# Performance work log

Measured on AMD Instinct MI355X. Metric: run time of the kernel, lower is better.

## Reference

```python
import jax, jax.numpy as jnp
import numpy as np

B, TQ, TKV, D, H = 2, 1024, 1024, 1024, 16
HD = D // H
BUCKETS, MAX_REL = 32, 128
SPAN = BUCKETS  # pos_ebd_size


def make_log_bucket_position(rel_pos, bucket_size, max_position):
    sign = jnp.sign(rel_pos)
    mid = bucket_size // 2
    abs_pos = jnp.where((rel_pos < mid) & (rel_pos > -mid), mid - 1, jnp.abs(rel_pos))
    log_pos = jnp.ceil(jnp.log(abs_pos.astype(jnp.float32) / mid)
                       / np.float32(np.log((max_position - 1) / mid)) * (mid - 1)) + mid
    return jnp.where(abs_pos <= mid, rel_pos, (log_pos * sign).astype(rel_pos.dtype))


def setup_inputs():
    key = jax.random.key(0)
    ks = jax.random.split(key, 12)
    s = 0.02
    f32 = jnp.float32
    return {
        "query_states": jax.random.normal(ks[0], (B, TQ, D), f32),
        "key_value_states": jax.random.normal(ks[1], (B, TKV, D), f32),
        "Wq": jax.random.normal(ks[2], (D, D), f32) * s, "bq": jnp.zeros((D,), f32),
        "Wk": jax.random.normal(ks[3], (D, D), f32) * s, "bk": jnp.zeros((D,), f32),
        "Wv": jax.random.normal(ks[4], (D, D), f32) * s, "bv": jnp.zeros((D,), f32),
        "Wo": jax.random.normal(ks[5], (D, D), f32) * s, "bo": jnp.zeros((D,), f32),
        "Wpk": jax.random.normal(ks[6], (D, D), f32) * s, "bpk": jnp.zeros((D,), f32),
        "Wpq": jax.random.normal(ks[7], (D, D), f32) * s, "bpq": jnp.zeros((D,), f32),
        "rel_emb": jax.random.normal(ks[8], (2 * SPAN, D), f32) * s,
        "ln_g": jnp.ones((D,), f32), "ln_b": jnp.zeros((D,), f32),
        "attention_mask": jnp.zeros((B, TKV), jnp.bool_),
    }


def reference(query_states, key_value_states, Wq, bq, Wk, bk, Wv, bv, Wo, bo,
              Wpk, bpk, Wpq, bpq, rel_emb, ln_g, ln_b, attention_mask):
    # projections -> [B,H,T,hd]
    q = (query_states @ Wq.T + bq).reshape(B, TQ, H, HD).transpose(0, 2, 1, 3)
    k = (key_value_states @ Wk.T + bk).reshape(B, TKV, H, HD).transpose(0, 2, 1, 3)
    v = (key_value_states @ Wv.T + bv).reshape(B, TKV, H, HD).transpose(0, 2, 1, 3)
    scale = jnp.sqrt(jnp.float32(HD * 3))  # scale_factor = 1 + c2p + p2c
    scores = jnp.einsum('bhqd,bhkd->bhqk', q, k) / scale

    # layer-normalized relative embeddings [2*SPAN, D]
    mu = rel_emb.mean(-1, keepdims=True)
    var = ((rel_emb - mu) ** 2).mean(-1, keepdims=True)
    re = (rel_emb - mu) * jax.lax.rsqrt(var + 1e-5) * ln_g + ln_b
    pos_k = (re @ Wpk.T + bpk).reshape(2 * SPAN, H, HD).transpose(1, 0, 2)  # [H,2S,hd]
    pos_q = (re @ Wpq.T + bpq).reshape(2 * SPAN, H, HD).transpose(1, 0, 2)

    rel = make_log_bucket_position(jnp.arange(TQ)[:, None] - jnp.arange(TKV)[None, :],
                                   BUCKETS, MAX_REL)                      # [Tq,Tkv]
    c2p_pos = jnp.clip(rel + SPAN, 0, 2 * SPAN - 1)
    p2c_pos = jnp.clip(-rel + SPAN, 0, 2 * SPAN - 1)
    pscale = jnp.sqrt(jnp.float32(HD * 2))

    # c2p: gather along relative-position axis
    c2p = jnp.einsum('bhqd,hpd->bhqp', q, pos_k)                          # [B,H,Tq,2S]
    iq = jnp.arange(TQ)[:, None]
    c2p_g = c2p[:, :, iq, c2p_pos]                                        # [B,H,Tq,Tkv]

    # p2c: gather then transpose (requires Tq == Tkv, as in original torch expand)
    p2c = jnp.einsum('bhkd,hpd->bhkp', k, pos_q)                          # [B,H,Tkv,2S]
    ik = jnp.arange(TKV)[:, None]
    p2c_g = p2c[:, :, ik, p2c_pos].transpose(0, 1, 3, 2)                  # [B,H,Tq,Tkv]

    scores = scores + c2p_g / pscale + p2c_g / pscale
    scores = jnp.where(attention_mask[:, None, None, :], -jnp.inf, scores)
    probs = jax.nn.softmax(scores.astype(jnp.float32), axis=-1).astype(q.dtype)

    ctx = jnp.einsum('bhqk,bhkd->bhqd', probs, v).transpose(0, 2, 1, 3).reshape(B, TQ, D)
    return ctx @ Wo.T + bo
```

## Files before the change

### kernel.cpp

```cpp
#include <hip/hip_runtime.h>
#include <hip/hip_bf16.h>
#include <math.h>

#define B   2
#define TQ  1024
#define TKV 1024
#define D   1024
#define H   16
#define HD  64
#define P   64
#define SPAN 32

#define NEG_INF (-3.0e38f)

typedef __attribute__((ext_vector_type(8))) short bf16x8;
typedef __attribute__((ext_vector_type(4))) float f32x4;
typedef unsigned short ushort_t;

static constexpr size_t QF_OFF   = 0;
static constexpr size_t RE_OFF   = (size_t)2 * 1024 * 1024;
static constexpr size_t POSK_OFF = RE_OFF + (size_t)64 * 1024;
static constexpr size_t POSQ_OFF = POSK_OFF + (size_t)64 * 1024;
static constexpr size_t FLOATS_END = POSQ_OFF + (size_t)64 * 1024;
static constexpr size_t SHORT_BASE_BYTES = FLOATS_END * 4;
static constexpr size_t C2P_S  = 0;
static constexpr size_t P2C_S  = (size_t)2 * 1024 * 1024;
static constexpr size_t KH_S   = (size_t)4 * 1024 * 1024;
static constexpr size_t KL_S   = (size_t)6 * 1024 * 1024;
static constexpr size_t VTH_S  = (size_t)8 * 1024 * 1024;
static constexpr size_t VTL_S  = (size_t)10 * 1024 * 1024;
static constexpr size_t CTXH_S = (size_t)12 * 1024 * 1024;
static constexpr size_t CTXL_S = (size_t)14 * 1024 * 1024;
static constexpr size_t TAB_OFF_BYTES = SHORT_BASE_BYTES + (size_t)16 * 1024 * 1024 * 2;

__device__ __forceinline__ void split2(float x, unsigned short& h, unsigned short& l) {
  unsigned int u = __float_as_uint(x);
  h = (unsigned short)(u >> 16);
  float r = x - __uint_as_float(u & 0xffff0000u);
  unsigned int v = __float_as_uint(r);
  v += 0x7fffu + ((v >> 16) & 1u);
  l = (unsigned short)(v >> 16);
}

__device__ __forceinline__ unsigned short bf16rn(float x) {
  unsigned int v = __float_as_uint(x);
  v += 0x7fffu + ((v >> 16) & 1u);
  return (unsigned short)(v >> 16);
}

__device__ __forceinline__ float bf2f(unsigned short u) {
  return __uint_as_float(((unsigned int)u) << 16);
}

__global__ __launch_bounds__(256) void ln_kernel(const float* __restrict__ x,
    const float* __restrict__ g, const float* __restrict__ bta, float* __restrict__ out) {
  const int row = blockIdx.x;
  const float* xr = x + (size_t)row * D;
  const int tid = threadIdx.x;
  __shared__ float red[4];
  float s = 0.f;
  for (int i = tid; i < D; i += 256) s += xr[i];
  #pragma unroll
  for (int off = 32; off; off >>= 1) s += __shfl_down(s, off);
  if ((tid & 63) == 0) red[tid >> 6] = s;
  __syncthreads();
  float mu = (red[0] + red[1] + red[2] + red[3]) * (1.0f / D);
  __syncthreads();
  float vs = 0.f;
  for (int i = tid; i < D; i += 256) { float dd = xr[i] - mu; vs += dd * dd; }
  #pragma unroll
  for (int off = 32; off; off >>= 1) vs += __shfl_down(vs, off);
  if ((tid & 63) == 0) red[tid >> 6] = vs;
  __syncthreads();
  float var = (red[0] + red[1] + red[2] + red[3]) * (1.0f / D);
  float rs = rsqrtf(var + 1e-5f);
  for (int i = tid; i < D; i += 256)
    out[(size_t)row * D + i] = (xr[i] - mu) * rs * g[i] + bta[i];
}

__global__ void tab_kernel(unsigned char* __restrict__ tab) {
  int i = blockIdx.x * 256 + threadIdx.x;
  if (i >= 2047) return;
  int d = i - 1023;
  int ad = d < 0 ? -d : d;
  int bucket;
  if (ad <= 16) {
    bucket = d;
  } else {
    double x = log((double)ad / 16.0) / log(127.0 / 16.0) * 15.0;
    double xr = floor(x + 0.5);
    double xc = (fabs(x - xr) < 1e-9) ? xr : ceil(x);
    int li = (int)xc + 16;
    bucket = (d > 0) ? li : -li;
  }
  int t = bucket + SPAN;
  t = t < 0 ? 0 : (t > 63 ? 63 : t);
  tab[i] = (unsigned char)t;
}

__global__ __launch_bounds__(256) void gemm_pos(const float* __restrict__ A,
    const float* __restrict__ W0, const float* __restrict__ b0, float* __restrict__ C0,
    const float* __restrict__ W1, const float* __restrict__ b1, float* __restrict__ C1) {
  const float* W = blockIdx.z ? W1 : W0;
  const float* bias = blockIdx.z ? b1 : b0;
  float* C = blockIdx.z ? C1 : C0;

  __shared__ short sAh[64 * 32], sAl[64 * 32], sBh[64 * 32], sBl[64 * 32];
  const int t = threadIdx.x;
  const int bn = blockIdx.x * 64;
  const int wid = t >> 6, lane = t & 63;
  const int wr = wid >> 1, wc = wid & 1;
  const int fr = lane & 15, fo = (lane >> 4) * 8;
  const int srow = t >> 3, scol = (t & 7) * 4;

  f32x4 acc[2][2];
  #pragma unroll
  for (int i = 0; i < 2; i++)
    #pragma unroll
    for (int j = 0; j < 2; j++) acc[i][j] = (f32x4){0.f, 0.f, 0.f, 0.f};

  float4 rA[2], rW[2];
  auto ld = [&](int k0) {
    #pragma unroll
    for (int i = 0; i < 2; i++) {
      rA[i] = *(const float4*)&A[(size_t)(srow + 32 * i) * 1024 + k0 + scol];
      rW[i] = *(const float4*)&W[(size_t)(bn + srow + 32 * i) * 1024 + k0 + scol];
    }
  };
  ld(0);

  for (int k0 = 0; k0 < 1024; k0 += 32) {
    __syncthreads();
    #pragma unroll
    for (int i = 0; i < 2; i++) {
      int row = srow + 32 * i;
      unsigned short h0,h1,h2,h3,l0,l1,l2,l3;
      split2(rA[i].x,h0,l0); split2(rA[i].y,h1,l1); split2(rA[i].z,h2,l2); split2(rA[i].w,h3,l3);
      *(short4*)&sAh[row * 32 + scol] = make_short4((short)h0,(short)h1,(short)h2,(short)h3);
      *(short4*)&sAl[row * 32 + scol] = make_short4((short)l0,(short)l1,(short)l2,(short)l3);
      split2(rW[i].x,h0,l0); split2(rW[i].y,h1,l1); split2(rW[i].z,h2,l2); split2(rW[i].w,h3,l3);
      *(short4*)&sBh[row * 32 + scol] = make_short4((short)h0,(short)h1,(short)h2,(short)h3);
      *(short4*)&sBl[row * 32 + scol] = make_short4((short)l0,(short)l1,(short)l2,(short)l3);
    }
    if (k0 + 32 < 1024) ld(k0 + 32);
    __syncthreads();

    bf16x8 ah[2], al[2], bh[2], bl[2];
    #pragma unroll
    for (int mf = 0; mf < 2; mf++) {
      int r = (wr * 32 + mf * 16 + fr) * 32 + fo;
      ah[mf] = *(const bf16x8*)&sAh[r];
      al[mf] = *(const bf16x8*)&sAl[r];
    }
    #pragma unroll
    for (int nf = 0; nf < 2; nf++) {
      int r = (wc * 32 + nf * 16 + fr) * 32 + fo;
      bh[nf] = *(const bf16x8*)&sBh[r];
      bl[nf] = *(const bf16x8*)&sBl[r];
    }
    #pragma unroll
    for (int mf = 0; mf < 2; mf++)
      #pragma unroll
      for (int nf = 0; nf < 2; nf++) {
        acc[mf][nf] = __builtin_amdgcn_mfma_f32_16x16x32_bf16(ah[mf], bh[nf], acc[mf][nf], 0, 0, 0);
        acc[mf][nf] = __builtin_amdgcn_mfma_f32_16x16x32_bf16(ah[mf], bl[nf], acc[mf][nf], 0, 0, 0);
        acc[mf][nf] = __builtin_amdgcn_mfma_f32_16x16x32_bf16(al[mf], bh[nf], acc[mf][nf], 0, 0, 0);
      }
  }

  #pragma unroll
  for (int mf = 0; mf < 2; mf++) {
    int rbase = wr * 32 + mf * 16 + (lane >> 4) * 4;
    #pragma unroll
    for (int nf = 0; nf < 2; nf++) {
      int col = bn + wc * 32 + nf * 16 + fr;
      float bb = bias[col];
      #pragma unroll
      for (int r = 0; r < 4; r++)
        C[(size_t)(rbase + r) * 1024 + col] = acc[mf][nf][r] + bb;
    }
  }
}

__global__ __launch_bounds__(256) void gemm_split(
    const float* __restrict__ A0, const float* __restrict__ A1, const float* __restrict__ A2,
    const float* __restrict__ W0, const float* __restrict__ W1, const float* __restrict__ W2,
    const float* __restrict__ b0, const float* __restrict__ b1, const float* __restrict__ b2,
    float* __restrict__ Cf0,
    ushort_t* __restrict__ KH_, ushort_t* __restrict__ KL_,
    ushort_t* __restrict__ VH_, ushort_t* __restrict__ VL_,
    int M, int N, int K) {
  const int z = blockIdx.z;
  const float* A = (z == 0) ? A0 : (z == 1) ? A1 : A2;
  const float* W = (z == 0) ? W0 : (z == 1) ? W1 : W2;
  const float* bias = (z == 0) ? b0 : (z == 1) ? b1 : b2;

  __shared__ short sAhi[128 * 32];
  __shared__ short sAlo[128 * 32];
  __shared__ short sBhi[64 * 32];
  __shared__ short sBlo[64 * 32];

  const int t = threadIdx.x;
  const int bm = blockIdx.y * 128, bn = blockIdx.x * 64;
  const int wid = t >> 6, lane = t & 63;
  const int wr = wid >> 1, wc = wid & 1;
  const int fr = lane & 15, fo = (lane >> 4) * 8;

  f32x4 acc[4][2];
  #pragma unroll
  for (int i = 0; i < 4; i++)
    #pragma unroll
    for (int j = 0; j < 2; j++)
      acc[i][j] = (f32x4){0.f, 0.f, 0.f, 0.f};

  const int srow = t >> 3;
  const int scol = (t & 7) * 4;

  float4 rA[4], rW[2];
  auto ld = [&](int k0) {
    #pragma unroll
    for (int i = 0; i < 4; i++)
      rA[i] = *(const float4*)&A[(size_t)(bm + srow + 32 * i) * K + k0 + scol];
    #pragma unroll
    for (int i = 0; i < 2; i++)
      rW[i] = *(const float4*)&W[(size_t)(bn + srow + 32 * i) * K + k0 + scol];
  };
  ld(0);

  for (int k0 = 0; k0 < K; k0 += 32) {
    __syncthreads();
    #pragma unroll
    for (int i = 0; i < 4; i++) {
      int row = srow + 32 * i;
      unsigned short h0, h1, h2, h3, l0, l1, l2, l3;
      split2(rA[i].x, h0, l0); split2(rA[i].y, h1, l1); split2(rA[i].z, h2, l2); split2(rA[i].w, h3, l3);
      *(short4*)&sAhi[row * 32 + scol] = make_short4((short)h0, (short)h1, (short)h2, (short)h3);
      *(short4*)&sAlo[row * 32 + scol] = make_short4((short)l0, (short)l1, (short)l2, (short)l3);
    }
    #pragma unroll
    for (int i = 0; i < 2; i++) {
      int row = srow + 32 * i;
      unsigned short h0, h1, h2, h3, l0, l1, l2, l3;
      split2(rW[i].x, h0, l0); split2(rW[i].y, h1, l1); split2(rW[i].z, h2, l2); split2(rW[i].w, h3, l3);
      *(short4*)&sBhi[row * 32 + scol] = make_short4((short)h0, (short)h1, (short)h2, (short)h3);
      *(short4*)&sBlo[row * 32 + scol] = make_short4((short)l0, (short)l1, (short)l2, (short)l3);
    }
    if (k0 + 32 < K) ld(k0 + 32);
    __syncthreads();

    bf16x8 ah[4], al[4], bh[2], bl[2];
    #pragma unroll
    for (int mf = 0; mf < 4; mf++) {
      int r = (wr * 64 + mf * 16 + fr) * 32 + fo;
      ah[mf] = *(const bf16x8*)&sAhi[r];
      al[mf] = *(const bf16x8*)&sAlo[r];
    }
    #pragma unroll
    for (int nf = 0; nf < 2; nf++) {
      int r = (wc * 32 + nf * 16 + fr) * 32 + fo;
      bh[nf] = *(const bf16x8*)&sBhi[r];
      bl[nf] = *(const bf16x8*)&sBlo[r];
    }
    #pragma unroll
    for (int mf = 0; mf < 4; mf++)
      #pragma unroll
      for (int nf = 0; nf < 2; nf++) {
        acc[mf][nf] = __builtin_amdgcn_mfma_f32_16x16x32_bf16(ah[mf], bh[nf], acc[mf][nf], 0, 0, 0);
        acc[mf][nf] = __builtin_amdgcn_mfma_f32_16x16x32_bf16(ah[mf], bl[nf], acc[mf][nf], 0, 0, 0);
        acc[mf][nf] = __builtin_amdgcn_mfma_f32_16x16x32_bf16(al[mf], bh[nf], acc[mf][nf], 0, 0, 0);
      }
  }

  if (z == 0) {
    #pragma unroll
    for (int mf = 0; mf < 4; mf++) {
      int rbase = bm + wr * 64 + mf * 16 + (lane >> 4) * 4;
      #pragma unroll
      for (int nf = 0; nf < 2; nf++) {
        int col = bn + wc * 32 + nf * 16 + fr;
        float bb = bias[col];
        #pragma unroll
        for (int r = 0; r < 4; r++)
          Cf0[(size_t)(rbase + r) * N + col] = acc[mf][nf][r] + bb;
      }
    }
  } else if (z == 1) {
    #pragma unroll
    for (int mf = 0; mf < 4; mf++) {
      int rbase = bm + wr * 64 + mf * 16 + (lane >> 4) * 4;
      #pragma unroll
      for (int nf = 0; nf < 2; nf++) {
        int col = bn + wc * 32 + nf * 16 + fr;
        float bb = bias[col];
        #pragma unroll
        for (int r = 0; r < 4; r++) {
          unsigned short hh, ll;
          split2(acc[mf][nf][r] + bb, hh, ll);
          KH_[(size_t)(rbase + r) * N + col] = hh;
          KL_[(size_t)(rbase + r) * N + col] = ll;
        }
      }
    }
  } else {
    #pragma unroll
    for (int mf = 0; mf < 4; mf++) {
      int m0 = bm + wr * 64 + mf * 16 + (lane >> 4) * 4;
      int bb2 = m0 >> 10, t0 = m0 & 1023;
      #pragma unroll
      for (int nf = 0; nf < 2; nf++) {
        int col = bn + wc * 32 + nf * 16 + fr;
        int hh = col >> 6, dd = col & 63;
        float bvv = bias[col];
        unsigned short h4[4], l4[4];
        #pragma unroll
        for (int r = 0; r < 4; r++) split2(acc[mf][nf][r] + bvv, h4[r], l4[r]);
        size_t dst = (((size_t)bb2 * 16 + hh) * 64 + dd) * 1024 + t0;
        *(short4*)&VH_[dst] = make_short4((short)h4[0], (short)h4[1], (short)h4[2], (short)h4[3]);
        *(short4*)&VL_[dst] = make_short4((short)l4[0], (short)l4[1], (short)l4[2], (short)l4[3]);
      }
    }
  }
}

__global__ __launch_bounds__(256) void gemm_out(
    const ushort_t* __restrict__ AH, const ushort_t* __restrict__ AL,
    const float* __restrict__ W, const float* __restrict__ bias, float* __restrict__ C) {
  __shared__ short sAh[64 * 32], sAl[64 * 32], sBh[64 * 32], sBl[64 * 32];
  const int t = threadIdx.x;
  const int bm = blockIdx.y * 64, bn = blockIdx.x * 64;
  const int wid = t >> 6, lane = t & 63;
  const int wr = wid >> 1, wc = wid & 1;
  const int fr = lane & 15, fo = (lane >> 4) * 8;
  const int arow = t >> 2, achk = (t & 3) * 8;
  const int srow = t >> 3, scol = (t & 7) * 4;

  f32x4 acc[2][2];
  #pragma unroll
  for (int i = 0; i < 2; i++)
    #pragma unroll
    for (int j = 0; j < 2; j++) acc[i][j] = (f32x4){0.f, 0.f, 0.f, 0.f};

  bf16x8 rAH, rAL;
  float4 rW[2];
  auto ld = [&](int k0) {
    rAH = *(const bf16x8*)&AH[(size_t)(bm + arow) * 1024 + k0 + achk];
    rAL = *(const bf16x8*)&AL[(size_t)(bm + arow) * 1024 + k0 + achk];
    #pragma unroll
    for (int i = 0; i < 2; i++)
      rW[i] = *(const float4*)&W[(size_t)(bn + srow + 32 * i) * 1024 + k0 + scol];
  };
  ld(0);

  for (int k0 = 0; k0 < 1024; k0 += 32) {
    __syncthreads();
    *(bf16x8*)&sAh[arow * 32 + achk] = rAH;
    *(bf16x8*)&sAl[arow * 32 + achk] = rAL;
    #pragma unroll
    for (int i = 0; i < 2; i++) {
      int row = srow + 32 * i;
      unsigned short h0,h1,h2,h3,l0,l1,l2,l3;
      split2(rW[i].x,h0,l0); split2(rW[i].y,h1,l1); split2(rW[i].z,h2,l2); split2(rW[i].w,h3,l3);
      *(short4*)&sBh[row * 32 + scol] = make_short4((short)h0,(short)h1,(short)h2,(short)h3);
      *(short4*)&sBl[row * 32 + scol] = make_short4((short)l0,(short)l1,(short)l2,(short)l3);
    }
    if (k0 + 32 < 1024) ld(k0 + 32);
    __syncthreads();

    bf16x8 ah[2], al[2], bh[2], bl[2];
    #pragma unroll
    for (int mf = 0; mf < 2; mf++) {
      int r = (wr * 32 + mf * 16 + fr) * 32 + fo;
      ah[mf] = *(const bf16x8*)&sAh[r];
      al[mf] = *(const bf16x8*)&sAl[r];
    }
    #pragma unroll
    for (int nf = 0; nf < 2; nf++) {
      int r = (wc * 32 + nf * 16 + fr) * 32 + fo;
      bh[nf] = *(const bf16x8*)&sBh[r];
      bl[nf] = *(const bf16x8*)&sBl[r];
    }
    #pragma unroll
    for (int mf = 0; mf < 2; mf++)
      #pragma unroll
      for (int nf = 0; nf < 2; nf++) {
        acc[mf][nf] = __builtin_amdgcn_mfma_f32_16x16x32_bf16(ah[mf], bh[nf], acc[mf][nf], 0, 0, 0);
        acc[mf][nf] = __builtin_amdgcn_mfma_f32_16x16x32_bf16(ah[mf], bl[nf], acc[mf][nf], 0, 0, 0);
        acc[mf][nf] = __builtin_amdgcn_mfma_f32_16x16x32_bf16(al[mf], bh[nf], acc[mf][nf], 0, 0, 0);
      }
  }

  #pragma unroll
  for (int mf = 0; mf < 2; mf++) {
    int rbase = bm + wr * 32 + mf * 16 + (lane >> 4) * 4;
    #pragma unroll
    for (int nf = 0; nf < 2; nf++) {
      int col = bn + wc * 32 + nf * 16 + fr;
      float bb = bias[col];
      #pragma unroll
      for (int r = 0; r < 4; r++)
        C[(size_t)(rbase + r) * 1024 + col] = acc[mf][nf][r] + bb;
    }
  }
}

__global__ __launch_bounds__(256) void relproj_kernel(
    const float* __restrict__ X0, const float* __restrict__ P0, ushort_t* __restrict__ O0,
    const ushort_t* __restrict__ XH1, const ushort_t* __restrict__ XL1,
    const float* __restrict__ P1, ushort_t* __restrict__ O1) {
  const int z = blockIdx.z;
  const float* POS = z ? P1 : P0;
  ushort_t* out = z ? O1 : O0;
  const int bh = blockIdx.y, b = bh >> 4, h = bh & 15;
  const int t0 = blockIdx.x * 64;
  __shared__ __align__(16) float sx[64][68];
  __shared__ __align__(16) float sp[64][68];
  const int tid = threadIdx.x;
  for (int i = tid; i < 4096; i += 256) {
    int r = i >> 6, d = i & 63;
    size_t idx = ((size_t)b * TQ + t0 + r) * D + h * HD + d;
    sx[d][r] = z ? (bf2f(XH1[idx]) + bf2f(XL1[idx])) : X0[idx];
    sp[d][r] = POS[(size_t)r * D + h * HD + d];
  }
  __syncthreads();
  const int tx = tid & 15, ty = tid >> 4;
  float acc[4][4] = {};
  for (int d = 0; d < 64; d++) {
    float4 a4 = *(const float4*)&sx[d][ty * 4];
    float4 b4 = *(const float4*)&sp[d][tx * 4];
    float av[4] = {a4.x, a4.y, a4.z, a4.w};
    float bv[4] = {b4.x, b4.y, b4.z, b4.w};
    #pragma unroll
    for (int i = 0; i < 4; i++)
      #pragma unroll
      for (int j = 0; j < 4; j++)
        acc[i][j] += av[i] * bv[j];
  }
  const float inv_ps = 0.08838834764831845f;
  #pragma unroll
  for (int i = 0; i < 4; i++)
    #pragma unroll
    for (int j = 0; j < 4; j++)
      out[((size_t)bh * TQ + t0 + ty * 4 + i) * P + tx * 4 + j] = bf16rn(acc[i][j] * inv_ps);
}

__global__ __launch_bounds__(256) void attn_mfma(
    const float* __restrict__ qb,
    const ushort_t* __restrict__ KH, const ushort_t* __restrict__ KL,
    const ushort_t* __restrict__ VTH, const ushort_t* __restrict__ VTL,
    const ushort_t* __restrict__ c2p, const ushort_t* __restrict__ p2c,
    const unsigned char* __restrict__ mask, const unsigned char* __restrict__ tab,
    ushort_t* __restrict__ CTXH, ushort_t* __restrict__ CTXL) {
  const int flat = blockIdx.y * gridDim.x + blockIdx.x;
  const int nid = (flat & 7) * 64 + (flat >> 3);
  const int bh = nid >> 4, b = bh >> 4, h = bh & 15;
  const int q0 = (nid & 15) * 64;

  const int tid = threadIdx.x;
  const int wid = tid >> 6, lane = tid & 63;
  const int g = lane >> 4, fr = lane & 15;

  __shared__ __align__(16) short sKh[4096], sKl[4096], sVh[4096], sVl[4096];
  __shared__ __align__(16) ushort_t sc2p[64][72];
  __shared__ __align__(16) ushort_t sp2c[64][72];
  __shared__ unsigned char stab[2048];
  __shared__ unsigned char smask[64];

  bf16x8 qh[2], ql[2];
  {
    const int qrow = q0 + wid * 16 + fr;
    const float* qp = qb + ((size_t)b * TQ + qrow) * D + h * HD + g * 8;
    #pragma unroll
    for (int ks = 0; ks < 2; ks++) {
      float4 x0 = *(const float4*)(qp + ks * 32);
      float4 x1 = *(const float4*)(qp + ks * 32 + 4);
      float xs[8] = {x0.x, x0.y, x0.z, x0.w, x1.x, x1.y, x1.z, x1.w};
      bf16x8 th, tl;
      #pragma unroll
      for (int j = 0; j < 8; j++) {
        unsigned short hh, ll;
        split2(xs[j], hh, ll);
        th[j] = (short)hh; tl[j] = (short)ll;
      }
      qh[ks] = th; ql[ks] = tl;
    }
  }

  const int sr = tid >> 2;
  const int sj0 = tid & 3;
  const int smf = sr >> 4, sfr = sr & 15;
  const int cb = (tid & 3) * 16;
  const int qloc = wid * 16 + fr;

  {
    const ushort_t* cp = c2p + ((size_t)bh * TQ + q0 + sr) * P + cb;
    *(bf16x8*)&sc2p[sr][cb]     = *(const bf16x8*)cp;
    *(bf16x8*)&sc2p[sr][cb + 8] = *(const bf16x8*)(cp + 8);
  }
  for (int i = tid; i < 2047; i += 256) stab[i] = tab[i];
  __syncthreads();
  const float c2p0  = bf2f(sc2p[qloc][0]);
  const float c2p63 = bf2f(sc2p[qloc][63]);

  f32x4 acc[4];
  #pragma unroll
  for (int nf = 0; nf < 4; nf++) acc[nf] = (f32x4){0.f, 0.f, 0.f, 0.f};
  float m_run = NEG_INF, l_run = 0.f;

  const float inv_s = 0.07216878364870323f;

  bf16x8 rKh[2], rKl[2], rVh[2], rVl[2], rP0, rP1;
  unsigned char rmask = 0;

  auto load_tile = [&](int kt) {
    const int k0n = kt * 64;
    const size_t kbase = ((size_t)b * TKV + k0n + sr) * D + h * HD;
    const size_t vbase = ((size_t)bh * HD + sr) * TKV + k0n;
    const ushort_t* pp = p2c + ((size_t)bh * TKV + k0n + sr) * P + cb;
    #pragma unroll
    for (int u = 0; u < 2; u++) {
      int jj = sj0 + u * 4;
      rKh[u] = *(const bf16x8*)(KH + kbase + jj * 8);
      rKl[u] = *(const bf16x8*)(KL + kbase + jj * 8);
      rVh[u] = *(const bf16x8*)(VTH + vbase + jj * 8);
      rVl[u] = *(const bf16x8*)(VTL + vbase + jj * 8);
    }
    rP0 = *(const bf16x8*)pp;
    rP1 = *(const bf16x8*)(pp + 8);
    if (tid < 64) rmask = mask[(size_t)b * TKV + k0n + tid];
  };

  load_tile(0);

  for (int kt = 0; kt < TKV / 64; kt++) {
    const int k0 = kt * 64;
    __syncthreads();
    #pragma unroll
    for (int u = 0; u < 2; u++) {
      int jj = sj0 + u * 4;
      int sub = smf * 8 + (jj >> 2) * 4 + (jj & 3);
      *(bf16x8*)&sKh[sub * 128 + sfr * 8] = rKh[u];
      *(bf16x8*)&sKl[sub * 128 + sfr * 8] = rKl[u];
      *(bf16x8*)&sVh[sub * 128 + sfr * 8] = rVh[u];
      *(bf16x8*)&sVl[sub * 128 + sfr * 8] = rVl[u];
    }
    *(bf16x8*)&sp2c[sr][cb]     = rP0;
    *(bf16x8*)&sp2c[sr][cb + 8] = rP1;
    if (tid < 64) smask[tid] = rmask;
    if (kt + 1 < TKV / 64) load_tile(kt + 1);
    __syncthreads();

    f32x4 st[4];
    #pragma unroll
    for (int mf = 0; mf < 4; mf++) st[mf] = (f32x4){0.f, 0.f, 0.f, 0.f};
    __builtin_amdgcn_s_setprio(1);
    #pragma unroll
    for (int mf = 0; mf < 4; mf++) {
      #pragma unroll
      for (int ks = 0; ks < 2; ks++) {
        bf16x8 kh = *(const bf16x8*)&sKh[(mf * 8 + ks * 4 + g) * 128 + fr * 8];
        bf16x8 kl = *(const bf16x8*)&sKl[(mf * 8 + ks * 4 + g) * 128 + fr * 8];
        st[mf] = __builtin_amdgcn_mfma_f32_16x16x32_bf16(kh, qh[ks], st[mf], 0, 0, 0);
        st[mf] = __builtin_amdgcn_mfma_f32_16x16x32_bf16(kh, ql[ks], st[mf], 0, 0, 0);
        st[mf] = __builtin_amdgcn_mfma_f32_16x16x32_bf16(kl, qh[ks], st[mf], 0, 0, 0);
      }
    }
    __builtin_amdgcn_s_setprio(0);

    const int dtile = q0 - k0;
    float pv[4][4];
    float lmax = NEG_INF;
    if (dtile >= 192 || dtile <= -192) {
      const int C = (dtile >= 192) ? 63 : 0;
      const float cbias = (dtile >= 192) ? c2p63 : c2p0;
      #pragma unroll
      for (int mf = 0; mf < 4; mf++) {
        #pragma unroll
        for (int rr = 0; rr < 4; rr++) {
          int kj = mf * 16 + g * 4 + rr;
          float v = st[mf][rr] * inv_s + (cbias + bf2f(sp2c[kj][C]));
          v = smask[kj] ? NEG_INF : v;
          pv[mf][rr] = v;
          lmax = fmaxf(lmax, v);
        }
      }
    } else {
      const int dq = q0 + qloc - k0 + 1023;
      const ushort_t* c2prow = &sc2p[qloc][0];
      #pragma unroll
      for (int mf = 0; mf < 4; mf++) {
        #pragma unroll
        for (int rr = 0; rr < 4; rr++) {
          int kj = mf * 16 + g * 4 + rr;
          int tbi = stab[dq - kj];
          float v = st[mf][rr] * inv_s + (bf2f(c2prow[tbi]) + bf2f(sp2c[kj][tbi]));
          v = smask[kj] ? NEG_INF : v;
          pv[mf][rr] = v;
          lmax = fmaxf(lmax, v);
        }
      }
    }
    lmax = fmaxf(lmax, __shfl_xor(lmax, 16));
    lmax = fmaxf(lmax, __shfl_xor(lmax, 32));
    if (!__all(lmax <= m_run)) {
      float mnew = fmaxf(m_run, lmax);
      float fac = __expf(m_run - mnew);
      m_run = mnew;
      l_run *= fac;
      float facr[4];
      #pragma unroll
      for (int rr = 0; rr < 4; rr++) facr[rr] = __shfl(fac, g * 4 + rr);
      #pragma unroll
      for (int nf = 0; nf < 4; nf++)
        #pragma unroll
        for (int rr = 0; rr < 4; rr++) acc[nf][rr] *= facr[rr];
    }
    float psum = 0.f;
    #pragma unroll
    for (int mf = 0; mf < 4; mf++)
      #pragma unroll
      for (int rr = 0; rr < 4; rr++) {
        float e = __expf(pv[mf][rr] - m_run);
        pv[mf][rr] = e;
        psum += e;
      }
    psum += __shfl_xor(psum, 16);
    psum += __shfl_xor(psum, 32);
    l_run += psum;

    bf16x8 pa[2];
    #pragma unroll
    for (int ks = 0; ks < 2; ks++) {
      bf16x8 t;
      #pragma unroll
      for (int j = 0; j < 8; j++) {
        int src = ((2 * (g & 1) + (j >> 2)) << 4) | fr;
        float v0 = __shfl(pv[2 * ks][j & 3], src);
        float v1 = __shfl(pv[2 * ks + 1][j & 3], src);
        float pvv = (g >> 1) ? v1 : v0;
        t[j] = (short)bf16rn(pvv);
      }
      pa[ks] = t;
    }

    __builtin_amdgcn_s_setprio(1);
    #pragma unroll
    for (int nf = 0; nf < 4; nf++) {
      #pragma unroll
      for (int ks = 0; ks < 2; ks++) {
        bf16x8 vh = *(const bf16x8*)&sVh[(nf * 8 + ks * 4 + g) * 128 + fr * 8];
        bf16x8 vl = *(const bf16x8*)&sVl[(nf * 8 + ks * 4 + g) * 128 + fr * 8];
        acc[nf] = __builtin_amdgcn_mfma_f32_16x16x32_bf16(pa[ks], vh, acc[nf], 0, 0, 0);
        acc[nf] = __builtin_amdgcn_mfma_f32_16x16x32_bf16(pa[ks], vl, acc[nf], 0, 0, 0);
      }
    }
    __builtin_amdgcn_s_setprio(0);
  }

  float invl[4];
  #pragma unroll
  for (int rr = 0; rr < 4; rr++) invl[rr] = 1.0f / __shfl(l_run, g * 4 + rr);
  #pragma unroll
  for (int nf = 0; nf < 4; nf++) {
    #pragma unroll
    for (int rr = 0; rr < 4; rr++) {
      int qrow = q0 + wid * 16 + g * 4 + rr;
      int dcol = h * HD + nf * 16 + fr;
      size_t idx = ((size_t)b * TQ + qrow) * D + dcol;
      unsigned short hh, ll;
      split2(acc[nf][rr] * invl[rr], hh, ll);
      CTXH[idx] = hh;
      CTXL[idx] = ll;
    }
  }
}

extern "C" void kernel_launch(void* const* d_in, const int* in_sizes, int n_in,
                              void* d_out, int out_size, void* d_ws, size_t ws_size,
                              hipStream_t stream) {
  const float* query = (const float*)d_in[0];
  const float* kv    = (const float*)d_in[1];
  const float* Wq  = (const float*)d_in[2];   const float* bq  = (const float*)d_in[3];
  const float* Wk  = (const float*)d_in[4];   const float* bk  = (const float*)d_in[5];
  const float* Wv  = (const float*)d_in[6];   const float* bv  = (const float*)d_in[7];
  const float* Wo  = (const float*)d_in[8];   const float* bo  = (const float*)d_in[9];
  const float* Wpk = (const float*)d_in[10];  const float* bpk = (const float*)d_in[11];
  const float* Wpq = (const float*)d_in[12];  const float* bpq = (const float*)d_in[13];
  const float* rel_emb = (const float*)d_in[14];
  const float* ln_g = (const float*)d_in[15];
  const float* ln_b = (const float*)d_in[16];
  const unsigned char* amask = (const unsigned char*)d_in[17];

  float* ws = (float*)d_ws;
  float* qbuf   = ws + QF_OFF;
  float* rebuf  = ws + RE_OFF;
  float* poskbuf = ws + POSK_OFF;
  float* posqbuf = ws + POSQ_OFF;
  ushort_t* sbase = (ushort_t*)((char*)d_ws + SHORT_BASE_BYTES);
  ushort_t* c2pbuf = sbase + C2P_S;
  ushort_t* p2cbuf = sbase + P2C_S;
  ushort_t* KH   = sbase + KH_S;
  ushort_t* KL   = sbase + KL_S;
  ushort_t* VTH  = sbase + VTH_S;
  ushort_t* VTL  = sbase + VTL_S;
  ushort_t* CTXH = sbase + CTXH_S;
  ushort_t* CTXL = sbase + CTXL_S;
  unsigned char* tab = (unsigned char*)d_ws + TAB_OFF_BYTES;

  ln_kernel<<<64, 256, 0, stream>>>(rel_emb, ln_g, ln_b, rebuf);
  tab_kernel<<<8, 256, 0, stream>>>(tab);
  gemm_pos<<<dim3(16, 1, 2), 256, 0, stream>>>(rebuf, Wpk, bpk, poskbuf, Wpq, bpq, posqbuf);
  gemm_split<<<dim3(16, 16, 3), 256, 0, stream>>>(
      query, kv, kv,  Wq, Wk, Wv,  bq, bk, bv,
      qbuf, KH, KL, VTH, VTL, 2048, 1024, 1024);
  relproj_kernel<<<dim3(16, 32, 2), 256, 0, stream>>>(
      qbuf, poskbuf, c2pbuf, KH, KL, posqbuf, p2cbuf);
  attn_mfma<<<dim3(16, 32), 256, 0, stream>>>(qbuf, KH, KL, VTH, VTL,
                                              c2pbuf, p2cbuf, amask, tab, CTXH, CTXL);
  gemm_out<<<dim3(16, 32), 256, 0, stream>>>(CTXH, CTXL, Wo, bo, (float*)d_out);
}
```

Before: 201.0 us.

## Presplit KV input to bf16 hi/lo, store Q split, remap GEMM block order

Adds a presplit kernel that converts key_value_states to bf16 hi/lo once, so the K and V projection blocks load pre-split operands instead of each splitting fp32 per tile. The Q projection now writes hi/lo bf16 directly, so the attention and relproj kernels load Q without re-splitting. Block indices in gemm_split and gemm_out are remapped, presumably to improve L2 reuse. This costs an extra launch and an extra read/write pass over kv, plus more workspace.

```diff
diff --git a/kernel.cpp b/kernel.cpp
--- a/kernel.cpp
+++ b/kernel.cpp
@@ -17,21 +17,24 @@
 typedef __attribute__((ext_vector_type(4))) float f32x4;
 typedef unsigned short ushort_t;
 
-static constexpr size_t QF_OFF   = 0;
-static constexpr size_t RE_OFF   = (size_t)2 * 1024 * 1024;
-static constexpr size_t POSK_OFF = RE_OFF + (size_t)64 * 1024;
-static constexpr size_t POSQ_OFF = POSK_OFF + (size_t)64 * 1024;
-static constexpr size_t FLOATS_END = POSQ_OFF + (size_t)64 * 1024;
+static constexpr size_t RE_OFF   = 0;
+static constexpr size_t POSK_OFF = (size_t)64 * 1024;
+static constexpr size_t POSQ_OFF = (size_t)128 * 1024;
+static constexpr size_t FLOATS_END = (size_t)192 * 1024;
 static constexpr size_t SHORT_BASE_BYTES = FLOATS_END * 4;
 static constexpr size_t C2P_S  = 0;
 static constexpr size_t P2C_S  = (size_t)2 * 1024 * 1024;
-static constexpr size_t KH_S   = (size_t)4 * 1024 * 1024;
-static constexpr size_t KL_S   = (size_t)6 * 1024 * 1024;
-static constexpr size_t VTH_S  = (size_t)8 * 1024 * 1024;
-static constexpr size_t VTL_S  = (size_t)10 * 1024 * 1024;
-static constexpr size_t CTXH_S = (size_t)12 * 1024 * 1024;
-static constexpr size_t CTXL_S = (size_t)14 * 1024 * 1024;
-static constexpr size_t TAB_OFF_BYTES = SHORT_BASE_BYTES + (size_t)16 * 1024 * 1024 * 2;
+static constexpr size_t QH_S   = (size_t)4 * 1024 * 1024;
+static constexpr size_t QL_S   = (size_t)6 * 1024 * 1024;
+static constexpr size_t KH_S   = (size_t)8 * 1024 * 1024;
+static constexpr size_t KL_S   = (size_t)10 * 1024 * 1024;
+static constexpr size_t VTH_S  = (size_t)12 * 1024 * 1024;
+static constexpr size_t VTL_S  = (size_t)14 * 1024 * 1024;
+static constexpr size_t CTXH_S = (size_t)16 * 1024 * 1024;
+static constexpr size_t CTXL_S = (size_t)18 * 1024 * 1024;
+static constexpr size_t AKVH_S = (size_t)20 * 1024 * 1024;
+static constexpr size_t AKVL_S = (size_t)22 * 1024 * 1024;
+static constexpr size_t TAB_OFF_BYTES = SHORT_BASE_BYTES + (size_t)24 * 1024 * 1024 * 2;
 
 __device__ __forceinline__ void split2(float x, unsigned short& h, unsigned short& l) {
   unsigned int u = __float_as_uint(x);
@@ -50,6 +53,23 @@
 
 __device__ __forceinline__ float bf2f(unsigned short u) {
   return __uint_as_float(((unsigned int)u) << 16);
+}
+
+__global__ __launch_bounds__(256) void presplit_kernel(const float* __restrict__ in,
+    ushort_t* __restrict__ oh, ushort_t* __restrict__ ol) {
+  size_t i = ((size_t)blockIdx.x * 256 + threadIdx.x) * 8;
+  float4 a = *(const float4*)&in[i];
+  float4 b = *(const float4*)&in[i + 4];
+  float xs[8] = {a.x, a.y, a.z, a.w, b.x, b.y, b.z, b.w};
+  bf16x8 th, tl;
+  #pragma unroll
+  for (int j = 0; j < 8; j++) {
+    unsigned short hh, ll;
+    split2(xs[j], hh, ll);
+    th[j] = (short)hh; tl[j] = (short)ll;
+  }
+  *(bf16x8*)&oh[i] = th;
+  *(bf16x8*)&ol[i] = tl;
 }
 
 __global__ __launch_bounds__(256) void ln_kernel(const float* __restrict__ x,
@@ -183,17 +203,22 @@
 }
 
 __global__ __launch_bounds__(256) void gemm_split(
-    const float* __restrict__ A0, const float* __restrict__ A1, const float* __restrict__ A2,
+    const float* __restrict__ Aq,
+    const ushort_t* __restrict__ AKVH, const ushort_t* __restrict__ AKVL,
     const float* __restrict__ W0, const float* __restrict__ W1, const float* __restrict__ W2,
     const float* __restrict__ b0, const float* __restrict__ b1, const float* __restrict__ b2,
-    float* __restrict__ Cf0,
+    ushort_t* __restrict__ QH_, ushort_t* __restrict__ QL_,
     ushort_t* __restrict__ KH_, ushort_t* __restrict__ KL_,
     ushort_t* __restrict__ VH_, ushort_t* __restrict__ VL_,
-    int M, int N, int K) {
+    int K) {
   const int z = blockIdx.z;
-  const float* A = (z == 0) ? A0 : (z == 1) ? A1 : A2;
   const float* W = (z == 0) ? W0 : (z == 1) ? W1 : W2;
   const float* bias = (z == 0) ? b0 : (z == 1) ? b1 : b2;
+
+  const int flat2 = blockIdx.y * 16 + blockIdx.x;
+  const int nid = (flat2 & 7) * 32 + (flat2 >> 3);
+  const int bn = (nid & 15) * 64;
+  const int bm = (nid >> 4) * 128;
 
   __shared__ short sAhi[128 * 32];
   __shared__ short sAlo[128 * 32];
@@ -201,7 +226,6 @@
   __shared__ short sBlo[64 * 32];
 
   const int t = threadIdx.x;
-  const int bm = blockIdx.y * 128, bn = blockIdx.x * 64;
   const int wid = t >> 6, lane = t & 63;
   const int wr = wid >> 1, wc = wid & 1;
   const int fr = lane & 15, fo = (lane >> 4) * 8;
@@ -215,12 +239,23 @@
 
   const int srow = t >> 3;
   const int scol = (t & 7) * 4;
+  const int ar = t >> 1;
+  const int ac = (t & 1) * 16;
 
   float4 rA[4], rW[2];
+  bf16x8 rAH[2], rAL[2];
   auto ld = [&](int k0) {
-    #pragma unroll
-    for (int i = 0; i < 4; i++)
-      rA[i] = *(const float4*)&A[(size_t)(bm + srow + 32 * i) * K + k0 + scol];
+    if (z == 0) {
+      #pragma unroll
+      for (int i = 0; i < 4; i++)
+        rA[i] = *(const float4*)&Aq[(size_t)(bm + srow + 32 * i) * K + k0 + scol];
+    } else {
+      const size_t abase = (size_t)(bm + ar) * K + k0 + ac;
+      rAH[0] = *(const bf16x8*)&AKVH[abase];
+      rAH[1] = *(const bf16x8*)&AKVH[abase + 8];
+      rAL[0] = *(const bf16x8*)&AKVL[abase];
+      rAL[1] = *(const bf16x8*)&AKVL[abase + 8];
+    }
     #pragma unroll
     for (int i = 0; i < 2; i++)
       rW[i] = *(const float4*)&W[(size_t)(bn + srow + 32 * i) * K + k0 + scol];
@@ -229,13 +264,20 @@
 
   for (int k0 = 0; k0 < K; k0 += 32) {
     __syncthreads();
-    #pragma unroll
-    for (int i = 0; i < 4; i++) {
-      int row = srow + 32 * i;
-      unsigned short h0, h1, h2, h3, l0, l1, l2, l3;
-      split2(rA[i].x, h0, l0); split2(rA[i].y, h1, l1); split2(rA[i].z, h2, l2); split2(rA[i].w, h3, l3);
-      *(short4*)&sAhi[row * 32 + scol] = make_short4((short)h0, (short)h1, (short)h2, (short)h3);
-      *(short4*)&sAlo[row * 32 + scol] = make_short4((short)l0, (short)l1, (short)l2, (short)l3);
+    if (z == 0) {
+      #pragma unroll
+      for (int i = 0; i < 4; i++) {
+        int row = srow + 32 * i;
+        unsigned short h0, h1, h2, h3, l0, l1, l2, l3;
+        split2(rA[i].x, h0, l0); split2(rA[i].y, h1, l1); split2(rA[i].z, h2, l2); split2(rA[i].w, h3, l3);
+        *(short4*)&sAhi[row * 32 + scol] = make_short4((short)h0, (short)h1, (short)h2, (short)h3);
+        *(short4*)&sAlo[row * 32 + scol] = make_short4((short)l0, (short)l1, (short)l2, (short)l3);
+      }
+    } else {
+      *(bf16x8*)&sAhi[ar * 32 + ac]     = rAH[0];
+      *(bf16x8*)&sAhi[ar * 32 + ac + 8] = rAH[1];
+      *(bf16x8*)&sAlo[ar * 32 + ac]     = rAL[0];
+      *(bf16x8*)&sAlo[ar * 32 + ac + 8] = rAL[1];
     }
     #pragma unroll
     for (int i = 0; i < 2; i++) {
@@ -271,37 +313,7 @@
       }
   }
 
-  if (z == 0) {
-    #pragma unroll
-    for (int mf = 0; mf < 4; mf++) {
-      int rbase = bm + wr * 64 + mf * 16 + (lane >> 4) * 4;
-      #pragma unroll
-      for (int nf = 0; nf < 2; nf++) {
-        int col = bn + wc * 32 + nf * 16 + fr;
-        float bb = bias[col];
-        #pragma unroll
-        for (int r = 0; r < 4; r++)
-          Cf0[(size_t)(rbase + r) * N + col] = acc[mf][nf][r] + bb;
-      }
-    }
-  } else if (z == 1) {
-    #pragma unroll
-    for (int mf = 0; mf < 4; mf++) {
-      int rbase = bm + wr * 64 + mf * 16 + (lane >> 4) * 4;
-      #pragma unroll
-      for (int nf = 0; nf < 2; nf++) {
-        int col = bn + wc * 32 + nf * 16 + fr;
-        float bb = bias[col];
-        #pragma unroll
-        for (int r = 0; r < 4; r++) {
-          unsigned short hh, ll;
-          split2(acc[mf][nf][r] + bb, hh, ll);
-          KH_[(size_t)(rbase + r) * N + col] = hh;
-          KL_[(size_t)(rbase + r) * N + col] = ll;
-        }
-      }
-    }
-  } else {
+  if (z == 2) {
     #pragma unroll
     for (int mf = 0; mf < 4; mf++) {
       int m0 = bm + wr * 64 + mf * 16 + (lane >> 4) * 4;
@@ -319,6 +331,25 @@
         *(short4*)&VL_[dst] = make_short4((short)l4[0], (short)l4[1], (short)l4[2], (short)l4[3]);
       }
     }
+  } else {
+    ushort_t* OH = (z == 0) ? QH_ : KH_;
+    ushort_t* OL = (z == 0) ? QL_ : KL_;
+    #pragma unroll
+    for (int mf = 0; mf < 4; mf++) {
+      int rbase = bm + wr * 64 + mf * 16 + (lane >> 4) * 4;
+      #pragma unroll
+      for (int nf = 0; nf < 2; nf++) {
+        int col = bn + wc * 32 + nf * 16 + fr;
+        float bb = bias[col];
+        #pragma unroll
+        for (int r = 0; r < 4; r++) {
+          unsigned short hh, ll;
+          split2(acc[mf][nf][r] + bb, hh, ll);
+          OH[(size_t)(rbase + r) * 1024 + col] = hh;
+          OL[(size_t)(rbase + r) * 1024 + col] = ll;
+        }
+      }
+    }
   }
 }
 
@@ -327,7 +358,10 @@
     const float* __restrict__ W, const float* __restrict__ bias, float* __restrict__ C) {
   __shared__ short sAh[64 * 32], sAl[64 * 32], sBh[64 * 32], sBl[64 * 32];
   const int t = threadIdx.x;
-  const int bm = blockIdx.y * 64, bn = blockIdx.x * 64;
+  const int flat2 = blockIdx.y * 16 + blockIdx.x;
+  const int nid = (flat2 & 7) * 64 + (flat2 >> 3);
+  const int bn = (nid & 15) * 64;
+  const int bm = (nid >> 4) * 64;
   const int wid = t >> 6, lane = t & 63;
   const int wr = wid >> 1, wc = wid & 1;
   const int fr = lane & 15, fo = (lane >> 4) * 8;
@@ -404,10 +438,13 @@
 }
 
 __global__ __launch_bounds__(256) void relproj_kernel(
-    const float* __restrict__ X0, const float* __restrict__ P0, ushort_t* __restrict__ O0,
+    const ushort_t* __restrict__ XH0, const ushort_t* __restrict__ XL0,
+    const float* __restrict__ P0, ushort_t* __restrict__ O0,
     const ushort_t* __restrict__ XH1, const ushort_t* __restrict__ XL1,
     const float* __restrict__ P1, ushort_t* __restrict__ O1) {
   const int z = blockIdx.z;
+  const ushort_t* XH = z ? XH1 : XH0;
+  const ushort_t* XL = z ? XL1 : XL0;
   const float* POS = z ? P1 : P0;
   ushort_t* out = z ? O1 : O0;
   const int bh = blockIdx.y, b = bh >> 4, h = bh & 15;
@@ -418,7 +455,7 @@
   for (int i = tid; i < 4096; i += 256) {
     int r = i >> 6, d = i & 63;
     size_t idx = ((size_t)b * TQ + t0 + r) * D + h * HD + d;
-    sx[d][r] = z ? (bf2f(XH1[idx]) + bf2f(XL1[idx])) : X0[idx];
+    sx[d][r] = bf2f(XH[idx]) + bf2f(XL[idx]);
     sp[d][r] = POS[(size_t)r * D + h * HD + d];
   }
   __syncthreads();
@@ -444,7 +481,7 @@
 }
 
 __global__ __launch_bounds__(256) void attn_mfma(
-    const float* __restrict__ qb,
+    const ushort_t* __restrict__ QHB, const ushort_t* __restrict__ QLB,
     const ushort_t* __restrict__ KH, const ushort_t* __restrict__ KL,
     const ushort_t* __restrict__ VTH, const ushort_t* __restrict__ VTL,
     const ushort_t* __restrict__ c2p, const ushort_t* __restrict__ p2c,
@@ -468,20 +505,11 @@
   bf16x8 qh[2], ql[2];
   {
     const int qrow = q0 + wid * 16 + fr;
-    const float* qp = qb + ((size_t)b * TQ + qrow) * D + h * HD + g * 8;
+    const size_t qidx = ((size_t)b * TQ + qrow) * D + h * HD + g * 8;
     #pragma unroll
     for (int ks = 0; ks < 2; ks++) {
-      float4 x0 = *(const float4*)(qp + ks * 32);
-      float4 x1 = *(const float4*)(qp + ks * 32 + 4);
-      float xs[8] = {x0.x, x0.y, x0.z, x0.w, x1.x, x1.y, x1.z, x1.w};
-      bf16x8 th, tl;
-      #pragma unroll
-      for (int j = 0; j < 8; j++) {
-        unsigned short hh, ll;
-        split2(xs[j], hh, ll);
-        th[j] = (short)hh; tl[j] = (short)ll;
-      }
-      qh[ks] = th; ql[ks] = tl;
+      qh[ks] = *(const bf16x8*)&QHB[qidx + ks * 32];
+      ql[ks] = *(const bf16x8*)&QLB[qidx + ks * 32];
     }
   }
 
@@ -691,30 +719,34 @@
   const unsigned char* amask = (const unsigned char*)d_in[17];
 
   float* ws = (float*)d_ws;
-  float* qbuf   = ws + QF_OFF;
-  float* rebuf  = ws + RE_OFF;
+  float* rebuf   = ws + RE_OFF;
   float* poskbuf = ws + POSK_OFF;
   float* posqbuf = ws + POSQ_OFF;
   ushort_t* sbase = (ushort_t*)((char*)d_ws + SHORT_BASE_BYTES);
   ushort_t* c2pbuf = sbase + C2P_S;
   ushort_t* p2cbuf = sbase + P2C_S;
+  ushort_t* QH   = sbase + QH_S;
+  ushort_t* QL   = sbase + QL_S;
   ushort_t* KH   = sbase + KH_S;
   ushort_t* KL   = sbase + KL_S;
   ushort_t* VTH  = sbase + VTH_S;
   ushort_t* VTL  = sbase + VTL_S;
   ushort_t* CTXH = sbase + CTXH_S;
   ushort_t* CTXL = sbase + CTXL_S;
+  ushort_t* AKVH = sbase + AKVH_S;
+  ushort_t* AKVL = sbase + AKVL_S;
   unsigned char* tab = (unsigned char*)d_ws + TAB_OFF_BYTES;
 
   ln_kernel<<<64, 256, 0, stream>>>(rel_emb, ln_g, ln_b, rebuf);
   tab_kernel<<<8, 256, 0, stream>>>(tab);
+  presplit_kernel<<<1024, 256, 0, stream>>>(kv, AKVH, AKVL);
   gemm_pos<<<dim3(16, 1, 2), 256, 0, stream>>>(rebuf, Wpk, bpk, poskbuf, Wpq, bpq, posqbuf);
   gemm_split<<<dim3(16, 16, 3), 256, 0, stream>>>(
-      query, kv, kv,  Wq, Wk, Wv,  bq, bk, bv,
-      qbuf, KH, KL, VTH, VTL, 2048, 1024, 1024);
+      query, AKVH, AKVL,  Wq, Wk, Wv,  bq, bk, bv,
+      QH, QL, KH, KL, VTH, VTL, 1024);
   relproj_kernel<<<dim3(16, 32, 2), 256, 0, stream>>>(
-      qbuf, poskbuf, c2pbuf, KH, KL, posqbuf, p2cbuf);
-  attn_mfma<<<dim3(16, 32), 256, 0, stream>>>(qbuf, KH, KL, VTH, VTL,
+      QH, QL, poskbuf, c2pbuf, KH, KL, posqbuf, p2cbuf);
+  attn_mfma<<<dim3(16, 32), 256, 0, stream>>>(QH, QL, KH, KL, VTH, VTL,
                                               c2pbuf, p2cbuf, amask, tab, CTXH, CTXL);
   gemm_out<<<dim3(16, 32), 256, 0, stream>>>(CTXH, CTXL, Wo, bo, (float*)d_out);
 }
```

New measurement: 199.4 us. No clear change (-0.8%).
